# Kernel optimization log

Measured on AMD Instinct MI355X. Metric: run time of the kernel, lower is better.

## Reference

```python
import jax, jax.numpy as jnp
import numpy as np

N = 100000      # nodes per graph
E = 1600000     # edges (avg degree 16)
T = 4           # time steps
NL = 15         # num_locations
FD = 3          # feature_dim_node
H, C = 2, 6     # heads, per-head channels (hidden_channels=12)
HC = H * C


def setup_inputs():
    key = jax.random.key(0)
    ks = jax.random.split(key, 24)
    inp = {
        'node_types': jax.random.randint(ks[0], (T, N), 0, 4, dtype=jnp.int32),
        'requests': jax.random.normal(ks[1], (T, N), jnp.float32),
        'time_index': jax.random.uniform(ks[2], (T, N), dtype=jnp.float32),
        'edge_index': jax.random.randint(ks[3], (T, 2, E), 0, N, dtype=jnp.int32),
        'emb': 0.1 * jax.random.normal(ks[4], (4, FD), jnp.float32),
    }
    dims = [FD + 2, HC, HC, HC]
    k = 5
    for i, din in enumerate(dims):
        inp[f'W{i}'] = jax.random.normal(ks[k], (din, HC), jnp.float32) / np.sqrt(din); k += 1
        inp[f'as{i}'] = 0.1 * jax.random.normal(ks[k], (H, C), jnp.float32); k += 1
        inp[f'ad{i}'] = 0.1 * jax.random.normal(ks[k], (H, C), jnp.float32); k += 1
        inp[f'b{i}'] = jnp.zeros((HC,), jnp.float32); k += 1
    return inp


def gat_layer(x, src, dst, W, a_s, a_d, b):
    # PyG GATConv: linear -> per-head additive attention -> softmax over incoming
    # edges (self-loops already appended to src/dst) -> weighted aggregation.
    h = (x @ W).reshape(N, H, C)
    e_s = (h * a_s).sum(-1)                                  # [N, H]
    e_d = (h * a_d).sum(-1)                                  # [N, H]
    logits = jax.nn.leaky_relu(e_s[src] + e_d[dst], 0.2)      # [E', H]
    m = jax.ops.segment_max(logits, dst, num_segments=N)
    m = jnp.where(jnp.isfinite(m), m, 0.0)
    p = jnp.exp(logits - m[dst])
    denom = jax.ops.segment_sum(p, dst, num_segments=N)
    alpha = p / (denom[dst] + 1e-16)
    out = jax.ops.segment_sum(alpha[:, :, None] * h[src], dst, num_segments=N)
    return out.reshape(N, HC) + b


def _forward(node_types, requests, time_index, edge_index, emb, params):
    def step(nt, req, ti, ei):
        x_emb = emb[nt]                                       # [N, FD]
        tail = req[NL:]
        mean = tail.mean()
        std = tail.std(ddof=1)                                # torch.std is unbiased
        req_f = jnp.concatenate([req[:NL], (tail - mean) / std])
        x = jnp.concatenate([x_emb, req_f[:, None], ti[:, None]], axis=-1)  # [N, FD+2]
        loops = jnp.arange(N, dtype=ei.dtype)
        src = jnp.concatenate([ei[0], loops])
        dst = jnp.concatenate([ei[1], loops])
        for i in range(3):                                     # att + 2 hidden_atts
            x = jax.nn.relu(gat_layer(x, src, dst, *params[i]))
        return gat_layer(x, src, dst, *params[3])              # final_att, no act
    return jax.vmap(step)(node_types, requests, time_index, edge_index)


def reference(node_types, requests, time_index, edge_index, emb,
              W0, as0, ad0, b0, W1, as1, ad1, b1,
              W2, as2, ad2, b2, W3, as3, ad3, b3):
    params = [(W0, as0, ad0, b0), (W1, as1, ad1, b1),
              (W2, as2, ad2, b2), (W3, as3, ad3, b3)]
    return _forward(node_types, requests, time_index, edge_index, emb, params)
```

## Files before the change

kernel.cpp:

```cpp
#include <hip/hip_runtime.h>
#include <hip/hip_fp16.h>
#include <math.h>

#define NN 100000
#define EE 1600000
#define TT 4
#define NLQ 15
#define FDQ 3
#define HCQ 12
#define CAP 48
#define RECU 8
#define NCB32 ((NN + 31) / 32)
#define BKT 512
#define NBKT ((NN + BKT - 1) / BKT)
#define EB 4096
#define NBE ((EE + EB - 1) / EB)
#define SPB 64

typedef int v4i __attribute__((ext_vector_type(4)));

__device__ __forceinline__ unsigned pack2(float a, float b) {
    __half2 h = __floats2half2_rn(a, b);
    return *reinterpret_cast<unsigned*>(&h);
}
__device__ __forceinline__ float2 unpack2(unsigned u) {
    __half2 h = *reinterpret_cast<__half2*>(&u);
    return __half22float2(h);
}

__global__ void statsA(const float* __restrict__ req, float* __restrict__ part) {
    int t = blockIdx.y, b = blockIdx.x;
    const float* r = req + (size_t)t * NN;
    const int NP = NN - NLQ;
    __shared__ float ssum[256], ssq[256];
    float s = 0.f, q = 0.f;
    for (int i = b * 256 + threadIdx.x; i < NP; i += SPB * 256) {
        float v = r[NLQ + i]; s += v; q += v * v;
    }
    ssum[threadIdx.x] = s; ssq[threadIdx.x] = q;
    __syncthreads();
    for (int off = 128; off > 0; off >>= 1) {
        if ((int)threadIdx.x < off) {
            ssum[threadIdx.x] += ssum[threadIdx.x + off];
            ssq[threadIdx.x]  += ssq[threadIdx.x + off];
        }
        __syncthreads();
    }
    if (threadIdx.x == 0) {
        part[(t * SPB + b) * 2]     = ssum[0];
        part[(t * SPB + b) * 2 + 1] = ssq[0];
    }
}

__global__ void statsB(const float* __restrict__ part, float* __restrict__ stats) {
    int t = blockIdx.x, k = threadIdx.x;
    __shared__ float ssum[64], ssq[64];
    ssum[k] = part[(t * SPB + k) * 2];
    ssq[k]  = part[(t * SPB + k) * 2 + 1];
    __syncthreads();
    for (int off = 32; off > 0; off >>= 1) {
        if (k < off) { ssum[k] += ssum[k + off]; ssq[k] += ssq[k + off]; }
        __syncthreads();
    }
    if (k == 0) {
        float n = (float)(NN - NLQ);
        float mean = ssum[0] / n;
        float var  = (ssq[0] - ssum[0] * mean) / (n - 1.0f);
        stats[t * 2]     = mean;
        stats[t * 2 + 1] = 1.0f / sqrtf(var);
    }
}

__global__ void histE(const int* __restrict__ ei, int* __restrict__ bh) {
    int t = blockIdx.y, b = blockIdx.x;
    __shared__ int h[NBKT];
    for (int i = threadIdx.x; i < NBKT; i += 256) h[i] = 0;
    __syncthreads();
    int base = b * EB;
    for (int k = 0; k < EB; k += 256) {
        int e = base + k + threadIdx.x;
        if (e < EE) {
            int dst = __builtin_nontemporal_load(ei + (size_t)t * 2 * EE + EE + e);
            atomicAdd(&h[dst >> 9], 1);
        }
    }
    __syncthreads();
    for (int i = threadIdx.x; i < NBKT; i += 256)
        bh[((size_t)t * NBE + b) * NBKT + i] = h[i];
}

__global__ void scanT(const int* __restrict__ bh, int* __restrict__ bhoff, int* __restrict__ tot) {
    int k = blockIdx.x, t = blockIdx.y;
    __shared__ int sv[512];
    int b = threadIdx.x;
    int v = (b < NBE) ? bh[((size_t)t * NBE + b) * NBKT + k] : 0;
    sv[b] = v;
    __syncthreads();
    for (int off = 1; off < 512; off <<= 1) {
        int x = (b >= off) ? sv[b - off] : 0;
        __syncthreads();
        sv[b] += x;
        __syncthreads();
    }
    if (b < NBE) bhoff[((size_t)t * NBE + b) * NBKT + k] = sv[b] - v;
    if (b == NBE - 1) tot[t * NBKT + k] = sv[b];
}

__global__ void baseT(const int* __restrict__ tot, int* __restrict__ bbase) {
    int t = blockIdx.x, k = threadIdx.x;
    __shared__ int sv[256];
    int v = (k < NBKT) ? tot[t * NBKT + k] : 0;
    sv[k] = v;
    __syncthreads();
    for (int off = 1; off < 256; off <<= 1) {
        int x = (k >= off) ? sv[k - off] : 0;
        __syncthreads();
        sv[k] += x;
        __syncthreads();
    }
    if (k < NBKT) bbase[t * (NBKT + 1) + k] = sv[k] - v;
    if (k == NBKT - 1) bbase[t * (NBKT + 1) + NBKT] = sv[k];
}

__global__ void scatE2(const int* __restrict__ ei, const int* __restrict__ bh,
                       const int* __restrict__ bhoff, const int* __restrict__ bbase,
                       unsigned* __restrict__ bke) {
    int t = blockIdx.y, b = blockIdx.x;
    __shared__ unsigned sorted[EB];
    __shared__ unsigned char bid[EB];
    __shared__ int loff[NBKT], cur[NBKT], goff[NBKT];
    __shared__ int sv[256];
    int k = threadIdx.x;
    int v = (k < NBKT) ? bh[((size_t)t * NBE + b) * NBKT + k] : 0;
    sv[k] = v;
    __syncthreads();
    for (int off = 1; off < 256; off <<= 1) {
        int x = (k >= off) ? sv[k - off] : 0;
        __syncthreads();
        sv[k] += x;
        __syncthreads();
    }
    if (k < NBKT) {
        int ex = sv[k] - v;
        loff[k] = ex;
        cur[k]  = ex;
        goff[k] = bbase[t * (NBKT + 1) + k]
                + bhoff[((size_t)t * NBE + b) * NBKT + k] - ex;
    }
    __syncthreads();
    int base = b * EB;
    int nvalid = (EE - base < EB) ? (EE - base) : EB;
    for (int e = threadIdx.x; e < nvalid; e += 256) {
        int src = __builtin_nontemporal_load(ei + (size_t)t * 2 * EE + base + e);
        int dst = __builtin_nontemporal_load(ei + (size_t)t * 2 * EE + EE + base + e);
        int bk = dst >> 9;
        int lp = atomicAdd(&cur[bk], 1);
        sorted[lp] = ((unsigned)(dst & 511) << 17) | (unsigned)src;
        bid[lp] = (unsigned char)bk;
    }
    __syncthreads();
    for (int p = threadIdx.x; p < nvalid; p += 256) {
        int B = bid[p];
        bke[(size_t)t * EE + goff[B] + p] = sorted[p];
    }
}

__global__ void fillv2(const unsigned* __restrict__ bke, const int* __restrict__ bbase,
                       int* __restrict__ cnt, int* __restrict__ csr) {
    extern __shared__ int sm[];
    int* cl    = sm;
    int* slots = sm + BKT;
    int t = blockIdx.y, b = blockIdx.x;
    int nbase = b * BKT;
    int nn = (NN - nbase < BKT) ? (NN - nbase) : BKT;
    for (int i = threadIdx.x; i < nn; i += 256) {
        cl[i] = 1;
        slots[i * CAP] = nbase + i;
    }
    __syncthreads();
    int beg = bbase[t * (NBKT + 1) + b], end = bbase[t * (NBKT + 1) + b + 1];
    const unsigned* bkt_ = bke + (size_t)t * EE;
    int nE = end - beg;
    for (int base0 = 0; base0 < nE; base0 += 1024) {
        unsigned pk[4];
#pragma unroll
        for (int j = 0; j < 4; j++) {
            int e = beg + base0 + j * 256 + threadIdx.x;
            pk[j] = (e < end) ? bkt_[e] : 0xFFFFFFFFu;
        }
#pragma unroll
        for (int j = 0; j < 4; j++) {
            if (pk[j] != 0xFFFFFFFFu) {
                int dl = pk[j] >> 17, src = (int)(pk[j] & 0x1FFFF);
                int pos = atomicAdd(&cl[dl], 1);
                slots[dl * CAP + pos] = src;
            }
        }
    }
    __syncthreads();
    const v4i* sl4 = (const v4i*)slots;
    v4i* dst4 = (v4i*)(csr + ((size_t)t * NN + nbase) * CAP);
    int tot4 = nn * CAP / 4;
    for (int i = threadIdx.x; i < tot4; i += 256)
        __builtin_nontemporal_store(sl4[i], dst4 + i);
    for (int i = threadIdx.x; i < nn; i += 256)
        cnt[t * NN + nbase + i] = cl[i];
}

__global__ void node0_kernel(const int* __restrict__ nt, const float* __restrict__ req,
                             const float* __restrict__ ti, const float* __restrict__ emb,
                             const float* __restrict__ W, const float* __restrict__ as_,
                             const float* __restrict__ ad_, const float* __restrict__ stats,
                             unsigned* __restrict__ hrec, float* __restrict__ ed) {
    __shared__ float sW[5 * HCQ], sas[HCQ], sad[HCQ];
    if (threadIdx.x < 5 * HCQ) sW[threadIdx.x] = W[threadIdx.x];
    if (threadIdx.x < HCQ) { sas[threadIdx.x] = as_[threadIdx.x]; sad[threadIdx.x] = ad_[threadIdx.x]; }
    __syncthreads();
    int id = blockIdx.x * blockDim.x + threadIdx.x;
    if (id >= TT * NN) return;
    int t = id / NN, n = id - t * NN;
    float mean = stats[t * 2], rstd = stats[t * 2 + 1];
    int typ = nt[id];
    float x[5];
    x[0] = emb[typ * FDQ + 0];
    x[1] = emb[typ * FDQ + 1];
    x[2] = emb[typ * FDQ + 2];
    float rv = req[id];
    x[3] = (n < NLQ) ? rv : (rv - mean) * rstd;
    x[4] = ti[id];
    float hv[HCQ];
#pragma unroll
    for (int c = 0; c < HCQ; c++) {
        float a = 0.f;
#pragma unroll
        for (int k = 0; k < 5; k++) a += x[k] * sW[k * HCQ + c];
        hv[c] = a;
    }
    float e0 = 0.f, e1 = 0.f, f0 = 0.f, f1 = 0.f;
#pragma unroll
    for (int c = 0; c < 6; c++) {
        e0 += hv[c] * sas[c];     f0 += hv[c] * sad[c];
        e1 += hv[6 + c] * sas[6 + c]; f1 += hv[6 + c] * sad[6 + c];
    }
    uint4* rp = (uint4*)(hrec + (size_t)id * RECU);
    rp[0] = make_uint4(pack2(hv[0], hv[1]), pack2(hv[2], hv[3]), pack2(hv[4], hv[5]), pack2(hv[6], hv[7]));
    rp[1] = make_uint4(pack2(hv[8], hv[9]), pack2(hv[10], hv[11]), __float_as_uint(e0), __float_as_uint(e1));
    ((float2*)ed)[id] = make_float2(f0, f1);
}

__global__ void edge_kernel(const int* __restrict__ cnt, const int* __restrict__ csr_src,
                            const unsigned* __restrict__ hrecI, const float* __restrict__ edI,
                            const float* __restrict__ bias,
                            const float* __restrict__ Wn, const float* __restrict__ asn,
                            const float* __restrict__ adn,
                            unsigned* __restrict__ hrecO, float* __restrict__ edO,
                            float* __restrict__ outF, int mode) {
    __shared__ float sb[HCQ], sW[HCQ * HCQ], sas[HCQ], sad[HCQ];
    if (threadIdx.x < HCQ) sb[threadIdx.x] = bias[threadIdx.x];
    if (mode == 0) {
        if (threadIdx.x < HCQ * HCQ) sW[threadIdx.x] = Wn[threadIdx.x];
        if (threadIdx.x < HCQ) { sas[threadIdx.x] = asn[threadIdx.x]; sad[threadIdx.x] = adn[threadIdx.x]; }
    }
    __syncthreads();
    int b = blockIdx.x;
    int t = b & 3;
    int nl = threadIdx.x >> 3, q = threadIdx.x & 7;
    int n = (b >> 2) * 32 + nl;
    if (n >= NN) return;
    int id = t * NN + n;
    int deg = cnt[id];
    const int*      srcs = csr_src + (size_t)id * CAP;
    const unsigned* hb   = hrecI + (size_t)t * NN * RECU;
    float2 edv = ((const float2*)edI)[id];
    float ed0 = edv.x, ed1 = edv.y;
    float d0 = 0.f, d1 = 0.f;
    float acc[HCQ];
#pragma unroll
    for (int c = 0; c < HCQ; c++) acc[c] = 0.f;

    auto process = [&](int4 s4, int ebase) {
        int rem = deg - ebase;
        int ss[4];
        ss[0] = s4.x;
        ss[1] = (rem > 1) ? s4.y : 0;
        ss[2] = (rem > 2) ? s4.z : 0;
        ss[3] = (rem > 3) ? s4.w : 0;
        uint4 ra[4], rb[4];
#pragma unroll
        for (int k = 0; k < 4; k++) {
            const uint4* hp = (const uint4*)(hb + (size_t)ss[k] * RECU);
            ra[k] = hp[0];
            rb[k] = hp[1];
        }
#pragma unroll
        for (int k = 0; k < 4; k++) {
            float valid = (rem > k) ? 1.0f : 0.0f;
            float l0 = __uint_as_float(rb[k].z) + ed0; l0 = fmaxf(l0, 0.2f * l0);
            float l1 = __uint_as_float(rb[k].w) + ed1; l1 = fmaxf(l1, 0.2f * l1);
            float w0 = __expf(l0) * valid, w1 = __expf(l1) * valid;
            d0 += w0; d1 += w1;
            float2 h01 = unpack2(ra[k].x), h23 = unpack2(ra[k].y), h45 = unpack2(ra[k].z);
            float2 h67 = unpack2(ra[k].w), h89 = unpack2(rb[k].x), hab = unpack2(rb[k].y);
            acc[0] += w0 * h01.x;  acc[1] += w0 * h01.y;
            acc[2] += w0 * h23.x;  acc[3] += w0 * h23.y;
            acc[4] += w0 * h45.x;  acc[5] += w0 * h45.y;
            acc[6] += w1 * h67.x;  acc[7] += w1 * h67.y;
            acc[8]  += w1 * h89.x; acc[9]  += w1 * h89.y;
            acc[10] += w1 * hab.x; acc[11] += w1 * hab.y;
        }
    };

    int e0s = q * 4;
    int4 sA = *(const int4*)(srcs + e0s);
    if (e0s < deg) process(sA, e0s);
    if (q < 4) {
        int e2 = 32 + q * 4;
        if (e2 < deg) {
            int4 sC = *(const int4*)(srcs + e2);
            process(sC, e2);
        }
    }

#pragma unroll
    for (int m = 1; m <= 4; m <<= 1) {
        d0 += __shfl_xor(d0, m);
        d1 += __shfl_xor(d1, m);
#pragma unroll
        for (int c = 0; c < HCQ; c++) acc[c] += __shfl_xor(acc[c], m);
    }

    float inv0 = 1.0f / (d0 + 1e-16f);
    float inv1 = 1.0f / (d1 + 1e-16f);
    float ov[HCQ];
#pragma unroll
    for (int c = 0; c < HCQ; c++)
        ov[c] = acc[c] * ((c < 6) ? inv0 : inv1) + sb[c];

    if (mode == 1) {
        if (q == 0) {
            float4* op = (float4*)(outF + (size_t)id * HCQ);
            op[0] = make_float4(ov[0], ov[1], ov[2], ov[3]);
            op[1] = make_float4(ov[4], ov[5], ov[6], ov[7]);
            op[2] = make_float4(ov[8], ov[9], ov[10], ov[11]);
        }
        return;
    }
    if (q >= 2) return;
#pragma unroll
    for (int c = 0; c < HCQ; c++) ov[c] = fmaxf(ov[c], 0.f);
    int base = q * 6;
    float hv[6];
#pragma unroll
    for (int j = 0; j < 6; j++) {
        float a = 0.f;
#pragma unroll
        for (int k = 0; k < HCQ; k++) a += ov[k] * sW[k * HCQ + base + j];
        hv[j] = a;
    }
    float ee = 0.f, ff = 0.f;
#pragma unroll
    for (int j = 0; j < 6; j++) { ee += hv[j] * sas[base + j]; ff += hv[j] * sad[base + j]; }
    unsigned w0 = pack2(hv[0], hv[1]);
    unsigned w1 = pack2(hv[2], hv[3]);
    unsigned w2 = pack2(hv[4], hv[5]);
    unsigned eeu = __float_as_uint(ee);
    unsigned send = (q == 0) ? eeu : w0;
    unsigned recv = __shfl_xor(send, 1);
    float fo = __shfl_xor(ff, 1);
    uint4* rp = (uint4*)(hrecO + (size_t)id * RECU);
    if (q == 0) {
        rp[0] = make_uint4(w0, w1, w2, recv);
        ((float2*)edO)[id] = make_float2(ff, fo);
    } else {
        rp[1] = make_uint4(w1, w2, recv, eeu);
    }
}

extern "C" void kernel_launch(void* const* d_in, const int* in_sizes, int n_in,
                              void* d_out, int out_size, void* d_ws, size_t ws_size,
                              hipStream_t stream) {
    const int*   nt  = (const int*)d_in[0];
    const float* req = (const float*)d_in[1];
    const float* ti  = (const float*)d_in[2];
    const int*   ei  = (const int*)d_in[3];
    const float* emb = (const float*)d_in[4];
    const float* W[4], *as_[4], *ad_[4], *bb[4];
    for (int l = 0; l < 4; l++) {
        W[l]   = (const float*)d_in[5 + l * 4 + 0];
        as_[l] = (const float*)d_in[5 + l * 4 + 1];
        ad_[l] = (const float*)d_in[5 + l * 4 + 2];
        bb[l]  = (const float*)d_in[5 + l * 4 + 3];
    }

    char* p = (char*)d_ws;
    auto alloc = [&](size_t bytes) -> void* {
        void* r = (void*)p;
        p += (bytes + 255) & ~(size_t)255;
        return r;
    };
    float*    stats = (float*)alloc((size_t)TT * 2 * 4);
    float*    part  = (float*)alloc((size_t)TT * SPB * 2 * 4);
    int*      cnt   = (int*)  alloc((size_t)TT * NN * 4);
    unsigned* hrecA = (unsigned*)alloc((size_t)TT * NN * RECU * 4);
    float*    edA   = (float*)alloc((size_t)TT * NN * 2 * 4);
    int*      bh    = (int*)  alloc((size_t)TT * NBE * NBKT * 4);
    int*      bhoff = (int*)  alloc((size_t)TT * NBE * NBKT * 4);
    int*      tot   = (int*)  alloc((size_t)TT * NBKT * 4);
    int*      bbase = (int*)  alloc((size_t)TT * (NBKT + 1) * 4);
    char*     ub    = (char*)alloc((size_t)TT * EE * 4);
    unsigned* bke   = (unsigned*)ub;
    unsigned* hrecB = (unsigned*)ub;
    float*    edB   = (float*)(ub + (size_t)TT * NN * RECU * 4);
    int*      csr   = (int*)  alloc((size_t)TT * NN * CAP * 4);

    statsA<<<dim3(SPB, TT), 256, 0, stream>>>(req, part);
    statsB<<<TT, 64, 0, stream>>>(part, stats);

    histE<<<dim3(NBE, TT), 256, 0, stream>>>(ei, bh);
    scanT<<<dim3(NBKT, TT), 512, 0, stream>>>(bh, bhoff, tot);
    baseT<<<TT, 256, 0, stream>>>(tot, bbase);
    scatE2<<<dim3(NBE, TT), 256, 0, stream>>>(ei, bh, bhoff, bbase, bke);
    size_t fillLds = (size_t)(BKT + BKT * CAP) * 4;
    fillv2<<<dim3(NBKT, TT), 256, fillLds, stream>>>(bke, bbase, cnt, csr);

    int ngrid = (TT * NN + 255) / 256;
    int egrid2 = 4 * NCB32;
    node0_kernel<<<ngrid, 256, 0, stream>>>(nt, req, ti, emb, W[0], as_[0], ad_[0], stats, hrecA, edA);
    edge_kernel<<<egrid2, 256, 0, stream>>>(cnt, csr, hrecA, edA, bb[0], W[1], as_[1], ad_[1],
                                            hrecB, edB, nullptr, 0);
    edge_kernel<<<egrid2, 256, 0, stream>>>(cnt, csr, hrecB, edB, bb[1], W[2], as_[2], ad_[2],
                                            hrecA, edA, nullptr, 0);
    edge_kernel<<<egrid2, 256, 0, stream>>>(cnt, csr, hrecA, edA, bb[2], W[3], as_[3], ad_[3],
                                            hrecB, edB, nullptr, 0);
    edge_kernel<<<egrid2, 256, 0, stream>>>(cnt, csr, hrecB, edB, bb[3], nullptr, nullptr, nullptr,
                                            nullptr, nullptr, (float*)d_out, 1);
}
```

Measured before the change: 453.6 us.

## Split edge aggregation per head with head-contiguous node records

```diff
diff --git a/kernel.cpp b/kernel.cpp
--- a/kernel.cpp
+++ b/kernel.cpp
@@ -10,7 +10,7 @@
 #define HCQ 12
 #define CAP 48
 #define RECU 8
-#define NCB32 ((NN + 31) / 32)
+#define NCB16 ((NN + 15) / 16)
 #define BKT 512
 #define NBKT ((NN + BKT - 1) / BKT)
 #define EB 4096
@@ -243,8 +243,8 @@
         e1 += hv[6 + c] * sas[6 + c]; f1 += hv[6 + c] * sad[6 + c];
     }
     uint4* rp = (uint4*)(hrec + (size_t)id * RECU);
-    rp[0] = make_uint4(pack2(hv[0], hv[1]), pack2(hv[2], hv[3]), pack2(hv[4], hv[5]), pack2(hv[6], hv[7]));
-    rp[1] = make_uint4(pack2(hv[8], hv[9]), pack2(hv[10], hv[11]), __float_as_uint(e0), __float_as_uint(e1));
+    rp[0] = make_uint4(pack2(hv[0], hv[1]), pack2(hv[2], hv[3]), pack2(hv[4], hv[5]), __float_as_uint(e0));
+    rp[1] = make_uint4(pack2(hv[6], hv[7]), pack2(hv[8], hv[9]), pack2(hv[10], hv[11]), __float_as_uint(e1));
     ((float2*)ed)[id] = make_float2(f0, f1);
 }
 
@@ -264,91 +264,90 @@
     __syncthreads();
     int b = blockIdx.x;
     int t = b & 3;
-    int nl = threadIdx.x >> 3, q = threadIdx.x & 7;
-    int n = (b >> 2) * 32 + nl;
+    int nl = threadIdx.x >> 4, q = threadIdx.x & 15;
+    int h  = q & 1;
+    int n = (b >> 2) * 16 + nl;
     if (n >= NN) return;
     int id = t * NN + n;
     int deg = cnt[id];
     const int*      srcs = csr_src + (size_t)id * CAP;
-    const unsigned* hb   = hrecI + (size_t)t * NN * RECU;
-    float2 edv = ((const float2*)edI)[id];
-    float ed0 = edv.x, ed1 = edv.y;
-    float d0 = 0.f, d1 = 0.f;
-    float acc[HCQ];
-#pragma unroll
-    for (int c = 0; c < HCQ; c++) acc[c] = 0.f;
-
-    auto process = [&](int4 s4, int ebase) {
+    const unsigned* hb   = hrecI + (size_t)t * NN * RECU + h * 4;
+    float edh = edI[2 * id + h];
+    float d = 0.f;
+    float acc[6];
+#pragma unroll
+    for (int c = 0; c < 6; c++) acc[c] = 0.f;
+
+    auto processH = [&](int4 s4, int ebase) {
         int rem = deg - ebase;
         int ss[4];
         ss[0] = s4.x;
         ss[1] = (rem > 1) ? s4.y : 0;
         ss[2] = (rem > 2) ? s4.z : 0;
         ss[3] = (rem > 3) ? s4.w : 0;
-        uint4 ra[4], rb[4];
-#pragma unroll
-        for (int k = 0; k < 4; k++) {
-            const uint4* hp = (const uint4*)(hb + (size_t)ss[k] * RECU);
-            ra[k] = hp[0];
-            rb[k] = hp[1];
-        }
+        uint4 r[4];
+#pragma unroll
+        for (int k = 0; k < 4; k++)
+            r[k] = *(const uint4*)(hb + (size_t)ss[k] * RECU);
 #pragma unroll
         for (int k = 0; k < 4; k++) {
             float valid = (rem > k) ? 1.0f : 0.0f;
-            float l0 = __uint_as_float(rb[k].z) + ed0; l0 = fmaxf(l0, 0.2f * l0);
-            float l1 = __uint_as_float(rb[k].w) + ed1; l1 = fmaxf(l1, 0.2f * l1);
-            float w0 = __expf(l0) * valid, w1 = __expf(l1) * valid;
-            d0 += w0; d1 += w1;
-            float2 h01 = unpack2(ra[k].x), h23 = unpack2(ra[k].y), h45 = unpack2(ra[k].z);
-            float2 h67 = unpack2(ra[k].w), h89 = unpack2(rb[k].x), hab = unpack2(rb[k].y);
-            acc[0] += w0 * h01.x;  acc[1] += w0 * h01.y;
-            acc[2] += w0 * h23.x;  acc[3] += w0 * h23.y;
-            acc[4] += w0 * h45.x;  acc[5] += w0 * h45.y;
-            acc[6] += w1 * h67.x;  acc[7] += w1 * h67.y;
-            acc[8]  += w1 * h89.x; acc[9]  += w1 * h89.y;
-            acc[10] += w1 * hab.x; acc[11] += w1 * hab.y;
+            float l = __uint_as_float(r[k].w) + edh; l = fmaxf(l, 0.2f * l);
+            float w = __expf(l) * valid;
+            d += w;
+            float2 h01 = unpack2(r[k].x), h23 = unpack2(r[k].y), h45 = unpack2(r[k].z);
+            acc[0] += w * h01.x;  acc[1] += w * h01.y;
+            acc[2] += w * h23.x;  acc[3] += w * h23.y;
+            acc[4] += w * h45.x;  acc[5] += w * h45.y;
         }
     };
 
-    int e0s = q * 4;
+    int e0s = (q >> 1) * 4;
     int4 sA = *(const int4*)(srcs + e0s);
-    if (e0s < deg) process(sA, e0s);
-    if (q < 4) {
-        int e2 = 32 + q * 4;
+    if (e0s < deg) processH(sA, e0s);
+    if (q < 8) {
+        int e2 = 32 + (q >> 1) * 4;
         if (e2 < deg) {
             int4 sC = *(const int4*)(srcs + e2);
-            process(sC, e2);
-        }
-    }
-
-#pragma unroll
-    for (int m = 1; m <= 4; m <<= 1) {
-        d0 += __shfl_xor(d0, m);
-        d1 += __shfl_xor(d1, m);
-#pragma unroll
-        for (int c = 0; c < HCQ; c++) acc[c] += __shfl_xor(acc[c], m);
-    }
-
-    float inv0 = 1.0f / (d0 + 1e-16f);
-    float inv1 = 1.0f / (d1 + 1e-16f);
+            processH(sC, e2);
+        }
+    }
+
+#pragma unroll
+    for (int m = 2; m <= 8; m <<= 1) {
+        d += __shfl_xor(d, m);
+#pragma unroll
+        for (int c = 0; c < 6; c++) acc[c] += __shfl_xor(acc[c], m);
+    }
+
+    float inv = 1.0f / (d + 1e-16f);
+    float ovl[6];
+#pragma unroll
+    for (int c = 0; c < 6; c++) ovl[c] = acc[c] * inv + sb[h * 6 + c];
+
+    if (mode == 1) {
+        if (q < 2) {
+            float* op = outF + (size_t)id * HCQ + h * 6;
+            if (h == 0) {
+                *(float4*)(op)     = make_float4(ovl[0], ovl[1], ovl[2], ovl[3]);
+                *(float2*)(op + 4) = make_float2(ovl[4], ovl[5]);
+            } else {
+                *(float2*)(op)     = make_float2(ovl[0], ovl[1]);
+                *(float4*)(op + 2) = make_float4(ovl[2], ovl[3], ovl[4], ovl[5]);
+            }
+        }
+        return;
+    }
+    float ovO[6];
+#pragma unroll
+    for (int c = 0; c < 6; c++) ovO[c] = __shfl_xor(ovl[c], 1);
+    if (q >= 2) return;
     float ov[HCQ];
 #pragma unroll
-    for (int c = 0; c < HCQ; c++)
-        ov[c] = acc[c] * ((c < 6) ? inv0 : inv1) + sb[c];
-
-    if (mode == 1) {
-        if (q == 0) {
-            float4* op = (float4*)(outF + (size_t)id * HCQ);
-            op[0] = make_float4(ov[0], ov[1], ov[2], ov[3]);
-            op[1] = make_float4(ov[4], ov[5], ov[6], ov[7]);
-            op[2] = make_float4(ov[8], ov[9], ov[10], ov[11]);
-        }
-        return;
-    }
-    if (q >= 2) return;
+    for (int c = 0; c < 6; c++) { ov[h * 6 + c] = ovl[c]; ov[(1 - h) * 6 + c] = ovO[c]; }
 #pragma unroll
     for (int c = 0; c < HCQ; c++) ov[c] = fmaxf(ov[c], 0.f);
-    int base = q * 6;
+    int base = h * 6;
     float hv[6];
 #pragma unroll
     for (int j = 0; j < 6; j++) {
@@ -360,20 +359,10 @@
     float ee = 0.f, ff = 0.f;
 #pragma unroll
     for (int j = 0; j < 6; j++) { ee += hv[j] * sas[base + j]; ff += hv[j] * sad[base + j]; }
-    unsigned w0 = pack2(hv[0], hv[1]);
-    unsigned w1 = pack2(hv[2], hv[3]);
-    unsigned w2 = pack2(hv[4], hv[5]);
-    unsigned eeu = __float_as_uint(ee);
-    unsigned send = (q == 0) ? eeu : w0;
-    unsigned recv = __shfl_xor(send, 1);
-    float fo = __shfl_xor(ff, 1);
-    uint4* rp = (uint4*)(hrecO + (size_t)id * RECU);
-    if (q == 0) {
-        rp[0] = make_uint4(w0, w1, w2, recv);
-        ((float2*)edO)[id] = make_float2(ff, fo);
-    } else {
-        rp[1] = make_uint4(w1, w2, recv, eeu);
-    }
+    uint4 rec = make_uint4(pack2(hv[0], hv[1]), pack2(hv[2], hv[3]), pack2(hv[4], hv[5]),
+                           __float_as_uint(ee));
+    ((uint4*)(hrecO + (size_t)id * RECU))[h] = rec;
+    edO[2 * id + h] = ff;
 }
 
 extern "C" void kernel_launch(void* const* d_in, const int* in_sizes, int n_in,
@@ -424,7 +413,7 @@
     fillv2<<<dim3(NBKT, TT), 256, fillLds, stream>>>(bke, bbase, cnt, csr);
 
     int ngrid = (TT * NN + 255) / 256;
-    int egrid2 = 4 * NCB32;
+    int egrid2 = 4 * NCB16;
     node0_kernel<<<ngrid, 256, 0, stream>>>(nt, req, ti, emb, W[0], as_[0], ad_[0], stats, hrecA, edA);
     edge_kernel<<<egrid2, 256, 0, stream>>>(cnt, csr, hrecA, edA, bb[0], W[1], as_[1], ad_[1],
                                             hrecB, edB, nullptr, 0);
```

Result: slower. 523.9 us (+15.5%).
